# Optimization experiments

Measured on AMD Instinct MI355X. Metric: run time of the kernel, lower is better.

Reference implementation:

```python
import jax, jax.numpy as jnp
import numpy as np

N, M, B, L, D = 100000, 256, 8, 128, 64
COORD_MAX = 1024


def setup_inputs() -> dict:
    key = jax.random.key(0)
    ks = jax.random.split(key, 9)
    # batch ids sorted so the original loop's centroid_offset == column index
    clu_b = jnp.sort(jax.random.randint(ks[0], (N, 1), 0, B))
    cen_b = jnp.sort(jax.random.randint(ks[1], (M, 1), 0, B))
    clu_xyz = jax.random.randint(ks[2], (N, 3), 0, COORD_MAX)
    cen_xyz = jax.random.randint(ks[3], (M, 3), 0, COORD_MAX)
    return {
        "cluster_coords": jnp.concatenate([clu_b, clu_xyz], axis=1).astype(jnp.int32),
        "centroid_coords": jnp.concatenate([cen_b, cen_xyz], axis=1).astype(jnp.int32),
        "cluster_feats": jax.random.normal(ks[4], (N, L), jnp.float32),
        "centroid_feats": jax.random.normal(ks[5], (M, L), jnp.float32),
        "centroid_conf": jax.random.uniform(ks[6], (M, 1), jnp.float32),
        "W": jax.random.normal(ks[7], (L, D), jnp.float32) * 0.05,
        "b": jax.random.normal(ks[8], (D,), jnp.float32) * 0.05,
    }


def reference(cluster_coords, centroid_coords, cluster_feats, centroid_feats,
              centroid_conf, W, b):
    # pointwise Conv3d(k=1) == linear on features
    clu = cluster_feats @ W + b                      # [N, D]
    nrm = jnp.maximum(jnp.linalg.norm(clu, axis=1, keepdims=True), 1e-12)
    clu = clu / nrm                                  # F.normalize(p=2, dim=1)
    cen = centroid_conf * (centroid_feats @ W + b)   # [M, D]

    # same-batch mask replaces the python loop + scatter
    valid = cluster_coords[:, 0][:, None] == centroid_coords[:, 0][None, :]  # [N, M]

    # pairwise L2 distance on spatial coords via squared expansion (exact for small ints)
    cc = cluster_coords[:, 1:].astype(jnp.float32)   # [N, 3]
    ec = centroid_coords[:, 1:].astype(jnp.float32)  # [M, 3]
    d2 = (jnp.sum(cc * cc, axis=1)[:, None]
          + jnp.sum(ec * ec, axis=1)[None, :]
          - 2.0 * cc @ ec.T)
    dist = jnp.maximum(jnp.sqrt(jnp.maximum(d2, 0.0)), 0.1)  # clamp(min=0.1)

    logits = jnp.where(valid, -dist, -jnp.inf)
    attn = jax.nn.softmax(logits, axis=-1)           # per-row over same-batch centroids
    attn = jnp.where(valid, attn, 0.0)               # rows w/ no centroids -> 0 (matches zeros init)

    out = (clu @ cen.T) * attn                       # [N, M]
    return out
```

## Files before the change

kernel.cpp:

```cpp
#include <hip/hip_runtime.h>
#include <stdint.h>


#define NN 100000
#define MM 256
#define LL 128
#define DD 64
#define NTILES (NN / 16)

typedef float f32x4 __attribute__((ext_vector_type(4)));
typedef __bf16 bf16x8 __attribute__((ext_vector_type(8)));

union U16x8 { uint4 u; bf16x8 v; unsigned short s[8]; };

static __device__ __forceinline__ unsigned short f2bf(float f) {
  union { float f; unsigned int i; } t; t.f = f;
  unsigned int x = t.i;
  x += 0x7fffu + ((x >> 16) & 1u);
  return (unsigned short)(x >> 16);
}

__global__ __launch_bounds__(256) void prep_kernel(
    const int* __restrict__ cen_coords,
    const float* __restrict__ cen_feats,
    const float* __restrict__ conf,
    const float* __restrict__ W,
    const float* __restrict__ bvec,
    unsigned short* __restrict__ cen_ws,
    unsigned short* __restrict__ wt_ws,
    float4* __restrict__ cmeta_ws)
{
  int tid = threadIdx.x;
  if (blockIdx.x < 16) {
    int m = blockIdx.x * 16 + (tid >> 4);
    int c = tid & 15;
    float a0 = 0.f, a1 = 0.f, a2 = 0.f, a3 = 0.f;
    for (int l = 0; l < LL; l++) {
      float f = cen_feats[m * LL + l];
      const float* wr = W + l * DD + c;
      a0 += f * wr[0];  a1 += f * wr[16];
      a2 += f * wr[32]; a3 += f * wr[48];
    }
    float cf = conf[m];
    cen_ws[m * DD + c +  0] = f2bf(cf * (a0 + bvec[c +  0]));
    cen_ws[m * DD + c + 16] = f2bf(cf * (a1 + bvec[c + 16]));
    cen_ws[m * DD + c + 32] = f2bf(cf * (a2 + bvec[c + 32]));
    cen_ws[m * DD + c + 48] = f2bf(cf * (a3 + bvec[c + 48]));
  } else {
    for (int i = tid; i < LL * DD; i += 256) {
      int l = i >> 6, d = i & 63;
      wt_ws[d * LL + l] = f2bf(W[l * DD + d]);
    }
    {
      int4 cc = ((const int4*)cen_coords)[tid];
      float4 f;
      f.x = (float)cc.y + 4096.0f * (float)cc.x;
      f.y = (float)cc.z;
      f.z = (float)cc.w;
      f.w = 0.0f;
      cmeta_ws[tid] = f;
    }
  }
}

__global__ __launch_bounds__(256) void main_kernel(
    const int4* __restrict__ clu_coords4,
    const float* __restrict__ feats,
    const float* __restrict__ bvec,
    const unsigned short* __restrict__ cen_ws,
    const unsigned short* __restrict__ wt_ws,
    const float4* __restrict__ cmeta,
    float* __restrict__ out)
{
  __shared__ __align__(16) unsigned short clu_s[4][16 * 72];

  int tid = threadIdx.x;
  int wave = tid >> 6, lane = tid & 63;
  int q = lane >> 4, c = lane & 15;
  int tile = blockIdx.x * 4 + wave;
  if (tile >= NTILES) return;

  f32x4 acc[4] = {{0,0,0,0},{0,0,0,0},{0,0,0,0},{0,0,0,0}};
  {
    const float4* fb = (const float4*)(feats + (size_t)(tile * 16 + c) * LL);
    const uint4* wb = (const uint4*)wt_ws;
#pragma unroll
    for (int ks = 0; ks < 4; ks++) {
      float4 f0 = fb[ks * 8 + q * 2];
      float4 f1 = fb[ks * 8 + q * 2 + 1];
      U16x8 a;
      a.s[0] = f2bf(f0.x); a.s[1] = f2bf(f0.y); a.s[2] = f2bf(f0.z); a.s[3] = f2bf(f0.w);
      a.s[4] = f2bf(f1.x); a.s[5] = f2bf(f1.y); a.s[6] = f2bf(f1.z); a.s[7] = f2bf(f1.w);
#pragma unroll
      for (int nt = 0; nt < 4; nt++) {
        U16x8 b; b.u = wb[(nt * 16 + c) * 16 + ks * 4 + q];
        acc[nt] = __builtin_amdgcn_mfma_f32_16x16x32_bf16(a.v, b.v, acc[nt], 0, 0, 0);
      }
    }
  }
#pragma unroll
  for (int nt = 0; nt < 4; nt++) {
    float bv = bvec[nt * 16 + c];
    acc[nt][0] += bv; acc[nt][1] += bv; acc[nt][2] += bv; acc[nt][3] += bv;
  }
  float inv_nrm[4];
#pragma unroll
  for (int r = 0; r < 4; r++) {
    float s = acc[0][r]*acc[0][r] + acc[1][r]*acc[1][r] + acc[2][r]*acc[2][r] + acc[3][r]*acc[3][r];
    s += __shfl_xor(s, 1); s += __shfl_xor(s, 2); s += __shfl_xor(s, 4); s += __shfl_xor(s, 8);
    inv_nrm[r] = 1.0f / fmaxf(sqrtf(s), 1e-12f);
  }
#pragma unroll
  for (int nt = 0; nt < 4; nt++)
#pragma unroll
    for (int r = 0; r < 4; r++)
      clu_s[wave][(q * 4 + r) * 72 + nt * 16 + c] = f2bf(acc[nt][r]);

  __builtin_amdgcn_sched_barrier(0);

  const uint4* cb = (const uint4*)(clu_s[wave]);
  U16x8 a0, a1;
  a0.u = cb[c * 9 + q];
  a1.u = cb[c * 9 + 4 + q];

  float rx[4], ry[4], rz[4];
#pragma unroll
  for (int r = 0; r < 4; r++) {
    int4 rm = clu_coords4[tile * 16 + q * 4 + r];
    rx[r] = (float)rm.y + 4096.0f * (float)rm.x;
    ry[r] = (float)rm.z;
    rz[r] = (float)rm.w;
  }

  float d2m[4] = {1e30f, 1e30f, 1e30f, 1e30f};
#pragma unroll
  for (int mt = 0; mt < 16; mt++) {
    float4 cm = cmeta[mt * 16 + c];
#pragma unroll
    for (int r = 0; r < 4; r++) {
      float dx = rx[r] - cm.x, dy = ry[r] - cm.y, dz = rz[r] - cm.z;
      float d2 = dx * dx + dy * dy + dz * dz;
      d2m[r] = fminf(d2m[r], d2);
    }
  }
  float dmv[4];
#pragma unroll
  for (int r = 0; r < 4; r++) {
    d2m[r] = fminf(d2m[r], __shfl_xor(d2m[r], 1));
    d2m[r] = fminf(d2m[r], __shfl_xor(d2m[r], 2));
    d2m[r] = fminf(d2m[r], __shfl_xor(d2m[r], 4));
    d2m[r] = fminf(d2m[r], __shfl_xor(d2m[r], 8));
    dmv[r] = fmaxf(sqrtf(d2m[r]), 0.1f);
  }

  float rsum[4] = {0.f, 0.f, 0.f, 0.f};
#pragma unroll
  for (int mt = 0; mt < 16; mt++) {
    float4 cm = cmeta[mt * 16 + c];
#pragma unroll
    for (int r = 0; r < 4; r++) {
      float dx = rx[r] - cm.x, dy = ry[r] - cm.y, dz = rz[r] - cm.z;
      float d = fmaxf(sqrtf(dx * dx + dy * dy + dz * dz), 0.1f);
      rsum[r] += __expf(dmv[r] - d);
    }
  }
  float scale[4];
#pragma unroll
  for (int r = 0; r < 4; r++) {
    rsum[r] += __shfl_xor(rsum[r], 1);
    rsum[r] += __shfl_xor(rsum[r], 2);
    rsum[r] += __shfl_xor(rsum[r], 4);
    rsum[r] += __shfl_xor(rsum[r], 8);
    scale[r] = (d2m[r] < 4.0e6f) ? inv_nrm[r] / rsum[r] : 0.f;
  }

  const uint4* cenb = (const uint4*)cen_ws;
  float* op[4];
#pragma unroll
  for (int r = 0; r < 4; r++)
    op[r] = out + (size_t)(tile * 16 + q * 4 + r) * MM + c;

#pragma unroll
  for (int mt = 0; mt < 16; mt++) {
    U16x8 b0, b1;
    b0.u = cenb[(mt * 16 + c) * 8 + q];
    b1.u = cenb[(mt * 16 + c) * 8 + 4 + q];
    f32x4 dacc = {0, 0, 0, 0};
    dacc = __builtin_amdgcn_mfma_f32_16x16x32_bf16(a0.v, b0.v, dacc, 0, 0, 0);
    dacc = __builtin_amdgcn_mfma_f32_16x16x32_bf16(a1.v, b1.v, dacc, 0, 0, 0);
    float4 cm = cmeta[mt * 16 + c];
#pragma unroll
    for (int r = 0; r < 4; r++) {
      float dx = rx[r] - cm.x, dy = ry[r] - cm.y, dz = rz[r] - cm.z;
      float d = fmaxf(sqrtf(dx * dx + dy * dy + dz * dz), 0.1f);
      float e = __expf(dmv[r] - d);
      op[r][mt * 16] = dacc[r] * (e * scale[r]);
    }
  }
}

extern "C" void kernel_launch(void* const* d_in, const int* in_sizes, int n_in,
                              void* d_out, int out_size, void* d_ws, size_t ws_size,
                              hipStream_t stream) {
  const int* clu_coords = (const int*)d_in[0];
  const int* cen_coords = (const int*)d_in[1];
  const float* clu_feats = (const float*)d_in[2];
  const float* cen_feats = (const float*)d_in[3];
  const float* conf      = (const float*)d_in[4];
  const float* W         = (const float*)d_in[5];
  const float* bvec      = (const float*)d_in[6];
  float* out = (float*)d_out;

  char* ws = (char*)d_ws;
  unsigned short* cen_ws = (unsigned short*)ws;
  unsigned short* wt_ws  = (unsigned short*)(ws + 32768);
  float4* cmeta_ws       = (float4*)(ws + 32768 + 16384);

  prep_kernel<<<17, 256, 0, stream>>>(cen_coords, cen_feats, conf, W, bvec,
                                      cen_ws, wt_ws, cmeta_ws);
  main_kernel<<<(NTILES + 3) / 4, 256, 0, stream>>>(
      (const int4*)clu_coords, clu_feats, bvec, cen_ws, wt_ws, cmeta_ws, out);
}
```

Measured before the change: 203.9 us.

## Split main kernel into GEMM and attention kernels, cache exp weights as fp16

```diff
diff --git a/kernel.cpp b/kernel.cpp
--- a/kernel.cpp
+++ b/kernel.cpp
@@ -10,8 +10,10 @@
 
 typedef float f32x4 __attribute__((ext_vector_type(4)));
 typedef __bf16 bf16x8 __attribute__((ext_vector_type(8)));
+typedef __fp16 fp16x2 __attribute__((ext_vector_type(2)));
 
 union U16x8 { uint4 u; bf16x8 v; unsigned short s[8]; };
+union UH2 { unsigned int u; fp16x2 h; };
 
 static __device__ __forceinline__ unsigned short f2bf(float f) {
   union { float f; unsigned int i; } t; t.f = f;
@@ -63,13 +65,10 @@
   }
 }
 
-__global__ __launch_bounds__(256) void main_kernel(
-    const int4* __restrict__ clu_coords4,
+__global__ __launch_bounds__(256, 8) void k1_gemm1(
     const float* __restrict__ feats,
     const float* __restrict__ bvec,
-    const unsigned short* __restrict__ cen_ws,
     const unsigned short* __restrict__ wt_ws,
-    const float4* __restrict__ cmeta,
     float* __restrict__ out)
 {
   __shared__ __align__(16) unsigned short clu_s[4][16 * 72];
@@ -89,8 +88,8 @@
       float4 f0 = fb[ks * 8 + q * 2];
       float4 f1 = fb[ks * 8 + q * 2 + 1];
       U16x8 a;
-      a.s[0] = f2bf(f0.x); a.s[1] = f2bf(f0.y); a.s[2] = f2bf(f0.z); a.s[3] = f2bf(f0.w);
-      a.s[4] = f2bf(f1.x); a.s[5] = f2bf(f1.y); a.s[6] = f2bf(f1.z); a.s[7] = f2bf(f1.w);
+      a.v[0] = (__bf16)f0.x; a.v[1] = (__bf16)f0.y; a.v[2] = (__bf16)f0.z; a.v[3] = (__bf16)f0.w;
+      a.v[4] = (__bf16)f1.x; a.v[5] = (__bf16)f1.y; a.v[6] = (__bf16)f1.z; a.v[7] = (__bf16)f1.w;
 #pragma unroll
       for (int nt = 0; nt < 4; nt++) {
         U16x8 b; b.u = wb[(nt * 16 + c) * 16 + ks * 4 + q];
@@ -113,15 +112,38 @@
 #pragma unroll
   for (int nt = 0; nt < 4; nt++)
 #pragma unroll
-    for (int r = 0; r < 4; r++)
-      clu_s[wave][(q * 4 + r) * 72 + nt * 16 + c] = f2bf(acc[nt][r]);
+    for (int r = 0; r < 4; r++) {
+      union { __bf16 h; unsigned short s; } u;
+      u.h = (__bf16)(acc[nt][r] * inv_nrm[r]);
+      clu_s[wave][(q * 4 + r) * 72 + nt * 16 + c] = u.s;
+    }
 
   __builtin_amdgcn_sched_barrier(0);
 
   const uint4* cb = (const uint4*)(clu_s[wave]);
+  uint4 s0 = cb[(lane >> 2) * 9 + (lane & 3) * 2];
+  uint4 s1 = cb[(lane >> 2) * 9 + (lane & 3) * 2 + 1];
+  uint4* stash = (uint4*)((char*)out + (size_t)tile * 16384);
+  stash[lane * 2]     = s0;
+  stash[lane * 2 + 1] = s1;
+}
+
+__global__ __launch_bounds__(256, 6) void k2_attn(
+    const int4* __restrict__ clu_coords4,
+    const unsigned short* __restrict__ cen_ws,
+    const float4* __restrict__ cmeta,
+    float* __restrict__ out)
+{
+  int tid = threadIdx.x;
+  int wave = tid >> 6, lane = tid & 63;
+  int q = lane >> 4, c = lane & 15;
+  int tile = blockIdx.x * 4 + wave;
+  if (tile >= NTILES) return;
+
+  const uint4* stash = (const uint4*)((const char*)out + (size_t)tile * 16384);
   U16x8 a0, a1;
-  a0.u = cb[c * 9 + q];
-  a1.u = cb[c * 9 + 4 + q];
+  a0.u = stash[c * 8 + q];
+  a1.u = stash[c * 8 + 4 + q];
 
   float rx[4], ry[4], rz[4];
 #pragma unroll
@@ -133,14 +155,13 @@
   }
 
   float d2m[4] = {1e30f, 1e30f, 1e30f, 1e30f};
-#pragma unroll
+#pragma unroll 4
   for (int mt = 0; mt < 16; mt++) {
     float4 cm = cmeta[mt * 16 + c];
 #pragma unroll
     for (int r = 0; r < 4; r++) {
       float dx = rx[r] - cm.x, dy = ry[r] - cm.y, dz = rz[r] - cm.z;
-      float d2 = dx * dx + dy * dy + dz * dz;
-      d2m[r] = fminf(d2m[r], d2);
+      d2m[r] = fminf(d2m[r], dx * dx + dy * dy + dz * dz);
     }
   }
   float dmv[4];
@@ -153,16 +174,24 @@
     dmv[r] = fmaxf(sqrtf(d2m[r]), 0.1f);
   }
 
+  uint2 ep[16];
   float rsum[4] = {0.f, 0.f, 0.f, 0.f};
 #pragma unroll
   for (int mt = 0; mt < 16; mt++) {
     float4 cm = cmeta[mt * 16 + c];
+    float e[4];
 #pragma unroll
     for (int r = 0; r < 4; r++) {
       float dx = rx[r] - cm.x, dy = ry[r] - cm.y, dz = rz[r] - cm.z;
       float d = fmaxf(sqrtf(dx * dx + dy * dy + dz * dz), 0.1f);
-      rsum[r] += __expf(dmv[r] - d);
-    }
+      e[r] = __expf(dmv[r] - d);
+      rsum[r] += e[r];
+    }
+    UH2 p0, p1;
+    p0.h = __builtin_amdgcn_cvt_pkrtz(e[0], e[1]);
+    p1.h = __builtin_amdgcn_cvt_pkrtz(e[2], e[3]);
+    ep[mt].x = p0.u;
+    ep[mt].y = p1.u;
   }
   float scale[4];
 #pragma unroll
@@ -171,15 +200,11 @@
     rsum[r] += __shfl_xor(rsum[r], 2);
     rsum[r] += __shfl_xor(rsum[r], 4);
     rsum[r] += __shfl_xor(rsum[r], 8);
-    scale[r] = (d2m[r] < 4.0e6f) ? inv_nrm[r] / rsum[r] : 0.f;
+    scale[r] = (d2m[r] < 4.0e6f) ? 1.0f / rsum[r] : 0.f;
   }
 
   const uint4* cenb = (const uint4*)cen_ws;
-  float* op[4];
-#pragma unroll
-  for (int r = 0; r < 4; r++)
-    op[r] = out + (size_t)(tile * 16 + q * 4 + r) * MM + c;
-
+  float* ob = out + (size_t)(tile * 16 + q * 4) * MM + c;
 #pragma unroll
   for (int mt = 0; mt < 16; mt++) {
     U16x8 b0, b1;
@@ -188,14 +213,11 @@
     f32x4 dacc = {0, 0, 0, 0};
     dacc = __builtin_amdgcn_mfma_f32_16x16x32_bf16(a0.v, b0.v, dacc, 0, 0, 0);
     dacc = __builtin_amdgcn_mfma_f32_16x16x32_bf16(a1.v, b1.v, dacc, 0, 0, 0);
-    float4 cm = cmeta[mt * 16 + c];
-#pragma unroll
-    for (int r = 0; r < 4; r++) {
-      float dx = rx[r] - cm.x, dy = ry[r] - cm.y, dz = rz[r] - cm.z;
-      float d = fmaxf(sqrtf(dx * dx + dy * dy + dz * dz), 0.1f);
-      float e = __expf(dmv[r] - d);
-      op[r][mt * 16] = dacc[r] * (e * scale[r]);
-    }
+    UH2 p0, p1; p0.u = ep[mt].x; p1.u = ep[mt].y;
+    ob[0 * MM + mt * 16] = dacc[0] * ((float)p0.h[0] * scale[0]);
+    ob[1 * MM + mt * 16] = dacc[1] * ((float)p0.h[1] * scale[1]);
+    ob[2 * MM + mt * 16] = dacc[2] * ((float)p1.h[0] * scale[2]);
+    ob[3 * MM + mt * 16] = dacc[3] * ((float)p1.h[1] * scale[3]);
   }
 }
 
@@ -218,6 +240,7 @@
 
   prep_kernel<<<17, 256, 0, stream>>>(cen_coords, cen_feats, conf, W, bvec,
                                       cen_ws, wt_ws, cmeta_ws);
-  main_kernel<<<(NTILES + 3) / 4, 256, 0, stream>>>(
-      (const int4*)clu_coords, clu_feats, bvec, cen_ws, wt_ws, cmeta_ws, out);
-}
+  int nblk = (NTILES + 3) / 4;
+  k1_gemm1<<<nblk, 256, 0, stream>>>(clu_feats, bvec, wt_ws, out);
+  k2_attn<<<nblk, 256, 0, stream>>>((const int4*)clu_coords, cen_ws, cmeta_ws, out);
+}
```

New measurement: 210.6 us. 1.03x slower.
